# Kernel tuning notes

Measured on AMD Instinct MI355X. Metric: run time of the kernel, lower is better.

The kernel has to match this reference:

```python
import jax, jax.numpy as jnp
import numpy as np

# dims: B=batch, S=src_len, H=hidden, E=char_embed, V=vocab, L=lstm layers
B, S, H, E, V, L = 512, 64, 1024, 256, 128, 2


def setup_inputs() -> dict:
    key = jax.random.key(0)
    ks = jax.random.split(key, 20)
    def n(k, shape, scale=0.05):
        return jax.random.normal(k, shape, dtype=jnp.float32) * scale
    return {
        "input_ids": jax.random.randint(ks[0], (B, 1), 0, V),
        "hidden": n(ks[1], (L, B, H), 1.0),
        "cell": n(ks[2], (L, B, H), 1.0),
        "encoder_outputs": n(ks[3], (B, S, H), 1.0),
        "emb": n(ks[4], (V, E)),          # nn.Embedding weight
        "U": n(ks[5], (H, H)),             # attention U (applied as x @ U)
        "W": n(ks[6], (H, H)),             # attention W
        "Vw": n(ks[7], (H, 1)),            # attention V -> scalar score
        "Wih0": n(ks[8], (4 * H, E + H)),  # LSTM layer0 input weights (i,f,g,o)
        "Whh0": n(ks[9], (4 * H, H)),
        "bih0": n(ks[10], (4 * H,)),
        "bhh0": n(ks[11], (4 * H,)),
        "Wih1": n(ks[12], (4 * H, H)),     # LSTM layer1
        "Whh1": n(ks[13], (4 * H, H)),
        "bih1": n(ks[14], (4 * H,)),
        "bhh1": n(ks[15], (4 * H,)),
        "out_w": n(ks[16], (V, H)),        # output nn.Linear weight (out,in)
        "out_b": n(ks[17], (V,)),
        "matrix": 0,
    }


def _lstm_step(x, h, c, Wih, Whh, bih, bhh):
    g = x @ Wih.T + h @ Whh.T + bih + bhh          # (B, 4H), torch gate order i,f,g,o
    i, f, gg, o = jnp.split(g, 4, axis=-1)
    c2 = jax.nn.sigmoid(f) * c + jax.nn.sigmoid(i) * jnp.tanh(gg)
    h2 = jax.nn.sigmoid(o) * jnp.tanh(c2)
    return h2, c2


def reference(input_ids, hidden, cell, encoder_outputs, emb, U, W, Vw,
              Wih0, Whh0, bih0, bhh0, Wih1, Whh1, bih1, bhh1,
              out_w, out_b, matrix):
    embedded = emb[input_ids]                                  # (B,1,E)
    t1 = jnp.einsum('bsh,hk->bsk', encoder_outputs, U)         # U(enc): (B,S,H)
    t2 = hidden[-1] @ W                                        # W(h_top): (B,H)
    e = jnp.tanh(t1 + t2[:, None, :]) @ Vw                     # scores: (B,S,1)
    a = jax.nn.softmax(e, axis=1)                              # attention weights over S
    ct = jnp.einsum('bso,bsh->boh', a, encoder_outputs)        # context: (B,1,H)
    x = jnp.concatenate([embedded, ct], axis=2)[:, 0, :]       # (B, E+H); dropout p=0 -> identity
    h0, c0 = _lstm_step(x, hidden[0], cell[0], Wih0, Whh0, bih0, bhh0)
    h1, c1 = _lstm_step(h0, hidden[1], cell[1], Wih1, Whh1, bih1, bhh1)
    out = (h1 @ out_w.T + out_b)[:, None, :]                   # (B,1,V)
    h_new = jnp.stack([h0, h1])
    c_new = jnp.stack([c0, c1])
    if matrix:
        return (a, out, h_new, c_new)
    return (out, h_new, c_new)
```

## Files before the change

### kernel.cpp

```cpp
#include <hip/hip_runtime.h>
#include <stdint.h>

#define BB 512
#define SS 64
#define HH 1024
#define EE 256
#define VV 128

typedef __attribute__((ext_vector_type(8))) short bf16x8;
typedef __attribute__((ext_vector_type(4))) float f32x4;

constexpr size_t OFF_ENC   = 0;
constexpr size_t OFF_WIH0  = OFF_ENC   + 67108864UL;
constexpr size_t OFF_WHH0  = OFF_WIH0  + 10485760UL;
constexpr size_t OFF_WIH1  = OFF_WHH0  + 8388608UL;
constexpr size_t OFF_WHH1  = OFF_WIH1  + 8388608UL;
constexpr size_t OFF_OUTW  = OFF_WHH1  + 8388608UL;
constexpr size_t OFF_HID0  = OFF_OUTW  + 262144UL;
constexpr size_t OFF_HLAST = OFF_HID0  + 1048576UL;
constexpr size_t OFF_UT    = OFF_HLAST + 1048576UL;
constexpr size_t OFF_WT    = OFF_UT    + 2097152UL;
constexpr size_t OFF_T2    = OFF_WT    + 2097152UL;
constexpr size_t OFF_E     = OFF_T2    + 2097152UL;
constexpr size_t OFF_EMB   = OFF_E     + 131072UL;
constexpr size_t OFF_CT    = OFF_EMB   + 262144UL;
constexpr size_t OFF_G     = OFF_CT    + 1048576UL;
constexpr size_t OFF_H0B   = OFF_G     + 8388608UL;
constexpr size_t OFF_H1B   = OFF_H0B   + 1048576UL;

__device__ __forceinline__ unsigned short f2bf(float f) {
  unsigned int u = __float_as_uint(f);
  unsigned int r = (u + 0x7FFFu + ((u >> 16) & 1u)) >> 16;
  return (unsigned short)r;
}
__device__ __forceinline__ float bf2f(unsigned short h) {
  return __uint_as_float(((unsigned int)h) << 16);
}

__device__ __forceinline__ void gload_lds16(const void* g, void* l) {
  __builtin_amdgcn_global_load_lds(
      (const __attribute__((address_space(1))) unsigned int*)g,
      (__attribute__((address_space(3))) unsigned int*)l, 16, 0, 0);
}

__global__ void cvt_all(const float* __restrict__ enc, const float* __restrict__ Wih0,
                        const float* __restrict__ Whh0, const float* __restrict__ Wih1,
                        const float* __restrict__ Whh1, const float* __restrict__ outw,
                        const float* __restrict__ hid, char* __restrict__ ws) {
  long i = (long)blockIdx.x * 256 + threadIdx.x;
  const long stride = (long)gridDim.x * 256;
  for (; i < 13139968L; i += stride) {
    const float4* src; ushort4* dst; long j;
    if (i < 8388608L)       { src = (const float4*)enc;  dst = (ushort4*)(ws + OFF_ENC);  j = i; }
    else if (i < 9699328L)  { src = (const float4*)Wih0; dst = (ushort4*)(ws + OFF_WIH0); j = i - 8388608L; }
    else if (i < 10747904L) { src = (const float4*)Whh0; dst = (ushort4*)(ws + OFF_WHH0); j = i - 9699328L; }
    else if (i < 11796480L) { src = (const float4*)Wih1; dst = (ushort4*)(ws + OFF_WIH1); j = i - 10747904L; }
    else if (i < 12845056L) { src = (const float4*)Whh1; dst = (ushort4*)(ws + OFF_WHH1); j = i - 11796480L; }
    else if (i < 12877824L) { src = (const float4*)outw; dst = (ushort4*)(ws + OFF_OUTW); j = i - 12845056L; }
    else if (i < 13008896L) { src = (const float4*)hid;  dst = (ushort4*)(ws + OFF_HID0); j = i - 12877824L; }
    else { src = (const float4*)(hid + 524288); dst = (ushort4*)(ws + OFF_HLAST); j = i - 13008896L; }
    float4 v = src[j];
    ushort4 o;
    o.x = f2bf(v.x); o.y = f2bf(v.y); o.z = f2bf(v.z); o.w = f2bf(v.w);
    dst[j] = o;
  }
}

__global__ void transpose_cvt2(const float* __restrict__ U, const float* __restrict__ W,
                               char* __restrict__ ws) {
  __shared__ float tile[32][33];
  const float* in = blockIdx.z ? W : U;
  unsigned short* out = (unsigned short*)(ws + (blockIdx.z ? OFF_WT : OFF_UT));
  int bc = blockIdx.x * 32, br = blockIdx.y * 32;
  int tx = threadIdx.x & 31, ty = threadIdx.x >> 5;
#pragma unroll
  for (int i = 0; i < 32; i += 8)
    tile[ty + i][tx] = in[(long)(br + ty + i) * HH + bc + tx];
  __syncthreads();
#pragma unroll
  for (int i = 0; i < 32; i += 8)
    out[(long)(bc + ty + i) * HH + br + tx] = f2bf(tile[tx][ty + i]);
}

__global__ void build_xemb(const int* __restrict__ ids, const float* __restrict__ emb,
                           unsigned short* __restrict__ embb) {
  int t = blockIdx.x * 256 + threadIdx.x;
  int b = t >> 6, c4 = t & 63;
  float4 v = ((const float4*)(emb + (long)ids[b] * 256))[c4];
  ushort4 o;
  o.x = f2bf(v.x); o.y = f2bf(v.y); o.z = f2bf(v.z); o.w = f2bf(v.w);
  ((ushort4*)embb)[t] = o;
}

__global__ __launch_bounds__(256) void gemm_seg(
    const unsigned short* __restrict__ A0, int KA0,
    const unsigned short* __restrict__ A1, int KA1,
    const unsigned short* __restrict__ A2,
    const unsigned short* __restrict__ B0, int KB0,
    const unsigned short* __restrict__ B1,
    float* __restrict__ C, int N, int Ktot) {
  __shared__ alignas(128) unsigned short lA[128 * 64];
  __shared__ alignas(128) unsigned short lB[64 * 64];
  const int tid = threadIdx.x;
  const int lane = tid & 63, wid = tid >> 6;
  const int wr = wid >> 1, wc = wid & 1;
  const int fr = lane & 15, fg = lane >> 4;
  f32x4 acc[4][2] = {};
  const long rowA0 = (long)blockIdx.x * 128;
  const long rowB0 = (long)blockIdx.y * 64;
  for (int kt = 0; kt < Ktot; kt += 64) {
    const unsigned short* Ap; int ka, lda;
    if (kt < KA0)            { Ap = A0; ka = kt;             lda = KA0; }
    else if (kt < KA0 + KA1) { Ap = A1; ka = kt - KA0;       lda = KA1; }
    else                     { Ap = A2; ka = kt - KA0 - KA1; lda = 1024; }
    const unsigned short* Bp; int kb, ldb;
    if (kt < KB0) { Bp = B0; kb = kt;       ldb = KB0; }
    else          { Bp = B1; kb = kt - KB0; ldb = 1024; }
#pragma unroll
    for (int j = 0; j < 4; ++j) {
      int c = j * 256 + tid;
      int r = c >> 3, cc = c & 7;
      int sc = cc ^ ((r >> 1) & 7);
      gload_lds16(Ap + (rowA0 + r) * (long)lda + ka + sc * 8, &lA[c * 8]);
    }
#pragma unroll
    for (int j = 0; j < 2; ++j) {
      int c = j * 256 + tid;
      int r = c >> 3, cc = c & 7;
      int sc = cc ^ ((r >> 1) & 7);
      gload_lds16(Bp + (rowB0 + r) * (long)ldb + kb + sc * 8, &lB[c * 8]);
    }
    __syncthreads();
#pragma unroll
    for (int kk = 0; kk < 64; kk += 32) {
      bf16x8 af[4], bfv[2];
#pragma unroll
      for (int m = 0; m < 4; ++m) {
        int row = wr * 64 + m * 16 + fr;
        int ch = ((kk >> 3) + fg) ^ ((row >> 1) & 7);
        af[m] = *(const bf16x8*)&lA[row * 64 + ch * 8];
      }
#pragma unroll
      for (int n = 0; n < 2; ++n) {
        int row = wc * 32 + n * 16 + fr;
        int ch = ((kk >> 3) + fg) ^ ((row >> 1) & 7);
        bfv[n] = *(const bf16x8*)&lB[row * 64 + ch * 8];
      }
#pragma unroll
      for (int m = 0; m < 4; ++m)
#pragma unroll
        for (int n = 0; n < 2; ++n)
          acc[m][n] = __builtin_amdgcn_mfma_f32_16x16x32_bf16(af[m], bfv[n],
                                                              acc[m][n], 0, 0, 0);
    }
    __syncthreads();
  }
#pragma unroll
  for (int m = 0; m < 4; ++m)
#pragma unroll
    for (int n = 0; n < 2; ++n)
#pragma unroll
      for (int r = 0; r < 4; ++r) {
        long grow = rowA0 + wr * 64 + m * 16 + fg * 4 + r;
        long gcol = rowB0 + wc * 32 + n * 16 + fr;
        C[grow * N + gcol] = acc[m][n][r];
      }
}

__global__ __launch_bounds__(256) void gemm_outproj(
    const unsigned short* __restrict__ A, const unsigned short* __restrict__ Bt,
    float* __restrict__ C) {
  __shared__ alignas(128) unsigned short lA[128 * 64];
  __shared__ alignas(128) unsigned short lB[128 * 64];
  const int tid = threadIdx.x;
  const int lane = tid & 63, wid = tid >> 6;
  const int wr = wid >> 1, wc = wid & 1;
  const int fr = lane & 15, fg = lane >> 4;
  f32x4 acc[4][4] = {};
  const long rowA0 = (long)blockIdx.x * 128;
  const int k0 = blockIdx.y * 128;
  for (int kt = k0; kt < k0 + 128; kt += 64) {
#pragma unroll
    for (int j = 0; j < 4; ++j) {
      int c = j * 256 + tid;
      int r = c >> 3, cc = c & 7;
      gload_lds16(A + (rowA0 + r) * 1024 + kt + cc * 8, &lA[c * 8]);
    }
#pragma unroll
    for (int j = 0; j < 4; ++j) {
      int c = j * 256 + tid;
      int r = c >> 3, cc = c & 7;
      gload_lds16(Bt + (long)r * 1024 + kt + cc * 8, &lB[c * 8]);
    }
    __syncthreads();
#pragma unroll
    for (int kk = 0; kk < 64; kk += 32) {
      bf16x8 af[4], bfv[4];
#pragma unroll
      for (int m = 0; m < 4; ++m)
        af[m] = *(const bf16x8*)&lA[(wr * 64 + m * 16 + fr) * 64 + kk + fg * 8];
#pragma unroll
      for (int n = 0; n < 4; ++n)
        bfv[n] = *(const bf16x8*)&lB[(wc * 64 + n * 16 + fr) * 64 + kk + fg * 8];
#pragma unroll
      for (int m = 0; m < 4; ++m)
#pragma unroll
        for (int n = 0; n < 4; ++n)
          acc[m][n] = __builtin_amdgcn_mfma_f32_16x16x32_bf16(af[m], bfv[n],
                                                              acc[m][n], 0, 0, 0);
    }
    __syncthreads();
  }
#pragma unroll
  for (int m = 0; m < 4; ++m)
#pragma unroll
    for (int n = 0; n < 4; ++n)
#pragma unroll
      for (int r = 0; r < 4; ++r) {
        long grow = rowA0 + wr * 64 + m * 16 + fg * 4 + r;
        long gcol = wc * 64 + n * 16 + fr;
        atomicAdd(&C[grow * 128 + gcol], acc[m][n][r]);
      }
}

__global__ void init_out_bias(const float* __restrict__ ob, float* __restrict__ out) {
  int i = blockIdx.x * 256 + threadIdx.x;
  out[i] = ob[i & 127];
}

__global__ __launch_bounds__(512, 2) void gemm_score256(
    const unsigned short* __restrict__ A, const unsigned short* __restrict__ Bt,
    const float* __restrict__ t2, const float* __restrict__ Vw,
    float* __restrict__ e) {
  extern __shared__ unsigned short smem[];
  const int K = HH;
  const int tid = threadIdx.x;
  const int lane = tid & 63, wid = tid >> 6;
  const int wr = wid >> 2;
  const int wcc = wid & 3;
  const int fr = lane & 15, fg = lane >> 4;
  int flat = blockIdx.y * 4 + blockIdx.x;
  int swz = (flat & 7) * 64 + (flat >> 3);
  const long rowA0 = (long)(swz >> 2) * 256;
  const long rowB0 = (long)(swz & 3) * 256;
  const int NKT = 16, NIT = 8;

  f32x4 acc[8][4] = {};

  auto RA = [&](int buf, int kh) { return (const unsigned short*)(smem + (buf * 4 + kh * 2) * 8192); };
  auto RB = [&](int buf, int kh) { return (const unsigned short*)(smem + (buf * 4 + kh * 2 + 1) * 8192); };

  auto stage = [&](int buf, int reg, int ktile) {
    const unsigned short* base = (reg & 1) ? Bt : A;
    long r0 = (reg & 1) ? rowB0 : rowA0;
    int kb = ktile * 64 + (reg >> 1) * 32;
    unsigned short* dst = smem + (buf * 4 + reg) * 8192;
#pragma unroll
    for (int j = 0; j < 2; ++j) {
      int c = j * 512 + tid;
      int row = c >> 2;
      int fgl = (c & 3) ^ ((row >> 1) & 3);
      gload_lds16(base + (r0 + row) * (long)K + kb + fgl * 8, dst + c * 8);
    }
  };
  auto readA = [&](const unsigned short* rg, int mh, bf16x8* af) {
#pragma unroll
    for (int m = 0; m < 4; ++m) {
      int row = wr * 128 + mh * 64 + m * 16 + fr;
      int slot = fg ^ ((row >> 1) & 3);
      af[m] = *(const bf16x8*)(rg + row * 32 + slot * 8);
    }
  };
  auto readB = [&](const unsigned short* rg, bf16x8* bv) {
#pragma unroll
    for (int n = 0; n < 4; ++n) {
      int row = wcc * 64 + n * 16 + fr;
      int slot = fg ^ ((row >> 1) & 3);
      bv[n] = *(const bf16x8*)(rg + row * 32 + slot * 8);
    }
  };
  auto mfma16 = [&](int mh, const bf16x8* af, const bf16x8* bv) {
    __builtin_amdgcn_s_setprio(1);
#pragma unroll
    for (int m = 0; m < 4; ++m)
#pragma unroll
      for (int n = 0; n < 4; ++n)
        acc[mh * 4 + m][n] = __builtin_amdgcn_mfma_f32_16x16x32_bf16(
            af[m], bv[n], acc[mh * 4 + m][n], 0, 0, 0);
    __builtin_amdgcn_s_setprio(0);
  };

#define BAR() __builtin_amdgcn_s_barrier()
#define WAIT6() asm volatile("s_waitcnt vmcnt(6)" ::: "memory")

  bf16x8 afA[4], afB[4], bvA[4], bvB[4];

  stage(0, 0, 0); stage(0, 1, 0); stage(0, 2, 0); stage(0, 3, 0);
  stage(1, 0, 1); stage(1, 1, 1);
  asm volatile("s_waitcnt vmcnt(8)" ::: "memory");
  BAR();
  readA(RA(0, 0), 0, afA); readB(RB(0, 0), bvA);

  for (int t = 0; t < NIT; ++t) {
    int k1 = 2 * t + 1, k2 = 2 * t + 2, k3 = 2 * t + 3;
    if (k2 >= NKT) k2 -= NKT;
    if (k3 >= NKT) k3 -= NKT;
    readA(RA(0, 0), 1, afB);
    stage(1, 2, k1);
    BAR(); mfma16(0, afA, bvA); BAR();
    WAIT6();
    readA(RA(0, 1), 0, afA); readB(RB(0, 1), bvB);
    stage(1, 3, k1);
    BAR(); mfma16(1, afB, bvA); BAR();
    readA(RA(0, 1), 1, afB);
    stage(0, 0, k2);
    BAR(); mfma16(0, afA, bvB); BAR();
    WAIT6();
    readA(RA(1, 0), 0, afA); readB(RB(1, 0), bvA);
    stage(0, 1, k2);
    BAR(); mfma16(1, afB, bvB); BAR();
    readA(RA(1, 0), 1, afB);
    stage(0, 2, k2);
    BAR(); mfma16(0, afA, bvA); BAR();
    WAIT6();
    readA(RA(1, 1), 0, afA); readB(RB(1, 1), bvB);
    stage(0, 3, k2);
    BAR(); mfma16(1, afB, bvA); BAR();
    readA(RA(1, 1), 1, afB);
    stage(1, 0, k3);
    BAR(); mfma16(0, afA, bvB); BAR();
    WAIT6();
    readA(RA(0, 0), 0, afA); readB(RB(0, 0), bvA);
    stage(1, 1, k3);
    BAR(); mfma16(1, afB, bvB); BAR();
  }
  asm volatile("s_waitcnt vmcnt(0)" ::: "memory");

  float t2v[2][4], vw[4];
#pragma unroll
  for (int n = 0; n < 4; ++n) {
    long col = rowB0 + wcc * 64 + n * 16 + fr;
    vw[n] = Vw[col];
#pragma unroll
    for (int h = 0; h < 2; ++h) {
      long b = (rowA0 >> 6) + wr * 2 + h;
      t2v[h][n] = t2[b * HH + col];
    }
  }
#pragma unroll
  for (int i = 0; i < 8; ++i) {
    int hsel = i >> 2;
    float part[4] = {0.f, 0.f, 0.f, 0.f};
#pragma unroll
    for (int n = 0; n < 4; ++n) {
#pragma unroll
      for (int r = 0; r < 4; ++r) {
        float tval = acc[i][n][r] + t2v[hsel][n];
        float th = 1.f - 2.f / (__expf(2.f * tval) + 1.f);
        part[r] += th * vw[n];
      }
    }
#pragma unroll
    for (int r = 0; r < 4; ++r) {
      float p = part[r];
      p += __shfl_xor(p, 1);
      p += __shfl_xor(p, 2);
      p += __shfl_xor(p, 4);
      p += __shfl_xor(p, 8);
      if (fr == 0)
        atomicAdd(&e[rowA0 + wr * 128 + i * 16 + fg * 4 + r], p);
    }
  }
#undef BAR
#undef WAIT6
}

__global__ void softmax_ctx(const float* __restrict__ e,
                            const unsigned short* __restrict__ encb,
                            unsigned short* __restrict__ ctb) {
  __shared__ float als[2][64];
  const int tid = threadIdx.x;
  const int bpair = blockIdx.x;
  if (tid < 128) {
    int b = bpair * 2 + (tid >> 6), s = tid & 63;
    float v = e[b * 64 + s];
    float mx = v;
#pragma unroll
    for (int o = 32; o; o >>= 1) mx = fmaxf(mx, __shfl_xor(mx, o));
    float ex = __expf(v - mx);
    float sm = ex;
#pragma unroll
    for (int o = 32; o; o >>= 1) sm += __shfl_xor(sm, o);
    als[tid >> 6][s] = ex / sm;
  }
  __syncthreads();
  int bi = tid >> 7, hg = tid & 127;
  int b = bpair * 2 + bi;
  const unsigned short* er = encb + (long)b * (SS * HH) + hg * 8;
  float s[8] = {0.f, 0.f, 0.f, 0.f, 0.f, 0.f, 0.f, 0.f};
  for (int i = 0; i < 64; ++i) {
    float av = als[bi][i];
    bf16x8 v = *(const bf16x8*)(er + (long)i * HH);
#pragma unroll
    for (int j = 0; j < 8; ++j) s[j] += av * bf2f((unsigned short)v[j]);
  }
  unsigned short* dst = ctb + (long)b * HH + hg * 8;
#pragma unroll
  for (int j = 0; j < 8; ++j) dst[j] = f2bf(s[j]);
}

__global__ void lstm_cell(const float* __restrict__ g, const float* __restrict__ bih,
                          const float* __restrict__ bhh, const float* __restrict__ cin,
                          float* __restrict__ hout, float* __restrict__ cout,
                          unsigned short* __restrict__ hb) {
  int idx = blockIdx.x * 256 + threadIdx.x;
  int b = idx >> 10, h = idx & 1023;
  const float* gr = g + (long)b * 4096;
  float gi = gr[h] + bih[h] + bhh[h];
  float gf = gr[1024 + h] + bih[1024 + h] + bhh[1024 + h];
  float gg = gr[2048 + h] + bih[2048 + h] + bhh[2048 + h];
  float go = gr[3072 + h] + bih[3072 + h] + bhh[3072 + h];
  float si = 1.f / (1.f + __expf(-gi));
  float sf = 1.f / (1.f + __expf(-gf));
  float so = 1.f / (1.f + __expf(-go));
  float tg = 1.f - 2.f / (__expf(2.f * gg) + 1.f);
  float c2 = sf * cin[idx] + si * tg;
  float tc = 1.f - 2.f / (__expf(2.f * c2) + 1.f);
  float h2 = so * tc;
  cout[idx] = c2;
  hout[idx] = h2;
  hb[idx] = f2bf(h2);
}

extern "C" void kernel_launch(void* const* d_in, const int* in_sizes, int n_in,
                              void* d_out, int out_size, void* d_ws, size_t ws_size,
                              hipStream_t stream) {
  const int* ids = (const int*)d_in[0];
  const float* hidden = (const float*)d_in[1];
  const float* cell = (const float*)d_in[2];
  const float* enc = (const float*)d_in[3];
  const float* emb = (const float*)d_in[4];
  const float* U = (const float*)d_in[5];
  const float* W = (const float*)d_in[6];
  const float* Vw = (const float*)d_in[7];
  const float* Wih0 = (const float*)d_in[8];
  const float* Whh0 = (const float*)d_in[9];
  const float* bih0 = (const float*)d_in[10];
  const float* bhh0 = (const float*)d_in[11];
  const float* Wih1 = (const float*)d_in[12];
  const float* Whh1 = (const float*)d_in[13];
  const float* bih1 = (const float*)d_in[14];
  const float* bhh1 = (const float*)d_in[15];
  const float* out_w = (const float*)d_in[16];
  const float* out_b = (const float*)d_in[17];
  float* out = (float*)d_out;
  char* ws = (char*)d_ws;
  (void)in_sizes; (void)n_in; (void)out_size; (void)ws_size;

  unsigned short* enc_b  = (unsigned short*)(ws + OFF_ENC);
  unsigned short* Wih0b  = (unsigned short*)(ws + OFF_WIH0);
  unsigned short* Whh0b  = (unsigned short*)(ws + OFF_WHH0);
  unsigned short* Wih1b  = (unsigned short*)(ws + OFF_WIH1);
  unsigned short* Whh1b  = (unsigned short*)(ws + OFF_WHH1);
  unsigned short* outwb  = (unsigned short*)(ws + OFF_OUTW);
  unsigned short* hid0b  = (unsigned short*)(ws + OFF_HID0);
  unsigned short* hlastb = (unsigned short*)(ws + OFF_HLAST);
  unsigned short* Utb    = (unsigned short*)(ws + OFF_UT);
  unsigned short* Wtb    = (unsigned short*)(ws + OFF_WT);
  float*          t2     = (float*)(ws + OFF_T2);
  float*          e      = (float*)(ws + OFF_E);
  unsigned short* embb   = (unsigned short*)(ws + OFF_EMB);
  unsigned short* ctb    = (unsigned short*)(ws + OFF_CT);
  float*          g      = (float*)(ws + OFF_G);
  unsigned short* h0b    = (unsigned short*)(ws + OFF_H0B);
  unsigned short* h1b    = (unsigned short*)(ws + OFF_H1B);

  float* out_logits = out;
  float* h_new = out + BB * VV;
  float* c_new = h_new + 2 * BB * HH;

  cvt_all<<<2048, 256, 0, stream>>>(enc, Wih0, Whh0, Wih1, Whh1, out_w, hidden, ws);
  transpose_cvt2<<<dim3(32, 32, 2), 256, 0, stream>>>(U, W, ws);
  build_xemb<<<128, 256, 0, stream>>>(ids, emb, embb);
  hipMemsetAsync(e, 0, (size_t)BB * SS * 4, stream);

  gemm_seg<<<dim3(4, 16), 256, 0, stream>>>(hlastb, 1024, nullptr, 0, nullptr,
                                            Wtb, 1024, nullptr, t2, HH, 1024);

  (void)hipFuncSetAttribute(reinterpret_cast<const void*>(gemm_score256),
                            hipFuncAttributeMaxDynamicSharedMemorySize, 131072);
  gemm_score256<<<dim3(4, 128), 512, 131072, stream>>>(enc_b, Utb, t2, Vw, e);

  softmax_ctx<<<256, 256, 0, stream>>>(e, enc_b, ctb);

  gemm_seg<<<dim3(4, 64), 256, 0, stream>>>(embb, 256, ctb, 1024, hid0b,
                                            Wih0b, 1280, Whh0b, g, 4 * HH, 2304);
  lstm_cell<<<BB * HH / 256, 256, 0, stream>>>(g, bih0, bhh0, cell, h_new, c_new, h0b);

  gemm_seg<<<dim3(4, 64), 256, 0, stream>>>(h0b, 1024, hlastb, 1024, nullptr,
                                            Wih1b, 1024, Whh1b, g, 4 * HH, 2048);
  lstm_cell<<<BB * HH / 256, 256, 0, stream>>>(g, bih1, bhh1, cell + BB * HH,
                                               h_new + BB * HH, c_new + BB * HH, h1b);

  init_out_bias<<<BB * VV / 256, 256, 0, stream>>>(out_b, out_logits);
  gemm_outproj<<<dim3(4, 8), 256, 0, stream>>>(h1b, outwb, out_logits);
}
```

Baseline: 256.9 us.

## Convert LSTM weights to bf16 inside GEMM loads and split-K the LSTM GEMMs

```diff
diff --git a/kernel.cpp b/kernel.cpp
--- a/kernel.cpp
+++ b/kernel.cpp
@@ -9,13 +9,10 @@
 
 typedef __attribute__((ext_vector_type(8))) short bf16x8;
 typedef __attribute__((ext_vector_type(4))) float f32x4;
+typedef __attribute__((ext_vector_type(8))) unsigned short u16x8;
 
 constexpr size_t OFF_ENC   = 0;
-constexpr size_t OFF_WIH0  = OFF_ENC   + 67108864UL;
-constexpr size_t OFF_WHH0  = OFF_WIH0  + 10485760UL;
-constexpr size_t OFF_WIH1  = OFF_WHH0  + 8388608UL;
-constexpr size_t OFF_WHH1  = OFF_WIH1  + 8388608UL;
-constexpr size_t OFF_OUTW  = OFF_WHH1  + 8388608UL;
+constexpr size_t OFF_OUTW  = OFF_ENC   + 67108864UL;
 constexpr size_t OFF_HID0  = OFF_OUTW  + 262144UL;
 constexpr size_t OFF_HLAST = OFF_HID0  + 1048576UL;
 constexpr size_t OFF_UT    = OFF_HLAST + 1048576UL;
@@ -36,6 +33,9 @@
 __device__ __forceinline__ float bf2f(unsigned short h) {
   return __uint_as_float(((unsigned int)h) << 16);
 }
+__device__ __forceinline__ unsigned int pkbf(float a, float b) {
+  return __builtin_amdgcn_perm(__float_as_uint(b), __float_as_uint(a), 0x07060302u);
+}
 
 __device__ __forceinline__ void gload_lds16(const void* g, void* l) {
   __builtin_amdgcn_global_load_lds(
@@ -43,27 +43,28 @@
       (__attribute__((address_space(3))) unsigned int*)l, 16, 0, 0);
 }
 
-__global__ void cvt_all(const float* __restrict__ enc, const float* __restrict__ Wih0,
-                        const float* __restrict__ Whh0, const float* __restrict__ Wih1,
-                        const float* __restrict__ Whh1, const float* __restrict__ outw,
-                        const float* __restrict__ hid, char* __restrict__ ws) {
+__global__ __launch_bounds__(256) void cvt_enc(const float* __restrict__ enc,
+                                               unsigned short* __restrict__ encb) {
   long i = (long)blockIdx.x * 256 + threadIdx.x;
-  const long stride = (long)gridDim.x * 256;
-  for (; i < 13139968L; i += stride) {
-    const float4* src; ushort4* dst; long j;
-    if (i < 8388608L)       { src = (const float4*)enc;  dst = (ushort4*)(ws + OFF_ENC);  j = i; }
-    else if (i < 9699328L)  { src = (const float4*)Wih0; dst = (ushort4*)(ws + OFF_WIH0); j = i - 8388608L; }
-    else if (i < 10747904L) { src = (const float4*)Whh0; dst = (ushort4*)(ws + OFF_WHH0); j = i - 9699328L; }
-    else if (i < 11796480L) { src = (const float4*)Wih1; dst = (ushort4*)(ws + OFF_WIH1); j = i - 10747904L; }
-    else if (i < 12845056L) { src = (const float4*)Whh1; dst = (ushort4*)(ws + OFF_WHH1); j = i - 11796480L; }
-    else if (i < 12877824L) { src = (const float4*)outw; dst = (ushort4*)(ws + OFF_OUTW); j = i - 12845056L; }
-    else if (i < 13008896L) { src = (const float4*)hid;  dst = (ushort4*)(ws + OFF_HID0); j = i - 12877824L; }
-    else { src = (const float4*)(hid + 524288); dst = (ushort4*)(ws + OFF_HLAST); j = i - 13008896L; }
-    float4 v = src[j];
-    ushort4 o;
-    o.x = f2bf(v.x); o.y = f2bf(v.y); o.z = f2bf(v.z); o.w = f2bf(v.w);
-    dst[j] = o;
-  }
+  float4 v = ((const float4*)enc)[i];
+  ushort4 o;
+  o.x = f2bf(v.x); o.y = f2bf(v.y); o.z = f2bf(v.z); o.w = f2bf(v.w);
+  ((ushort4*)encb)[i] = o;
+}
+
+__global__ __launch_bounds__(256) void cvt_small(const float* __restrict__ hid,
+                                                 const float* __restrict__ outw,
+                                                 char* __restrict__ ws) {
+  int i = blockIdx.x * 256 + threadIdx.x;
+  const float4* src;
+  ushort4* dst;
+  int j;
+  if (i < 262144) { src = (const float4*)hid;  dst = (ushort4*)(ws + OFF_HID0); j = i; }
+  else            { src = (const float4*)outw; dst = (ushort4*)(ws + OFF_OUTW); j = i - 262144; }
+  float4 v = src[j];
+  ushort4 o;
+  o.x = f2bf(v.x); o.y = f2bf(v.y); o.z = f2bf(v.z); o.w = f2bf(v.w);
+  dst[j] = o;
 }
 
 __global__ void transpose_cvt2(const float* __restrict__ U, const float* __restrict__ W,
@@ -92,13 +93,13 @@
   ((ushort4*)embb)[t] = o;
 }
 
+template <int BF32>
 __global__ __launch_bounds__(256) void gemm_seg(
     const unsigned short* __restrict__ A0, int KA0,
     const unsigned short* __restrict__ A1, int KA1,
     const unsigned short* __restrict__ A2,
-    const unsigned short* __restrict__ B0, int KB0,
-    const unsigned short* __restrict__ B1,
-    float* __restrict__ C, int N, int Ktot) {
+    const void* __restrict__ B0v, int KB0, const void* __restrict__ B1v,
+    float* __restrict__ C0p, float* __restrict__ C1p, int N, int Ktot, int Khalf) {
   __shared__ alignas(128) unsigned short lA[128 * 64];
   __shared__ alignas(128) unsigned short lB[64 * 64];
   const int tid = threadIdx.x;
@@ -108,27 +109,54 @@
   f32x4 acc[4][2] = {};
   const long rowA0 = (long)blockIdx.x * 128;
   const long rowB0 = (long)blockIdx.y * 64;
-  for (int kt = 0; kt < Ktot; kt += 64) {
+  const int ktb = blockIdx.z * Khalf;
+  int kte = ktb + Khalf; if (kte > Ktot) kte = Ktot;
+  float* C = blockIdx.z ? C1p : C0p;
+  for (int kt = ktb; kt < kte; kt += 64) {
     const unsigned short* Ap; int ka, lda;
     if (kt < KA0)            { Ap = A0; ka = kt;             lda = KA0; }
     else if (kt < KA0 + KA1) { Ap = A1; ka = kt - KA0;       lda = KA1; }
     else                     { Ap = A2; ka = kt - KA0 - KA1; lda = 1024; }
-    const unsigned short* Bp; int kb, ldb;
-    if (kt < KB0) { Bp = B0; kb = kt;       ldb = KB0; }
-    else          { Bp = B1; kb = kt - KB0; ldb = 1024; }
-#pragma unroll
-    for (int j = 0; j < 4; ++j) {
-      int c = j * 256 + tid;
-      int r = c >> 3, cc = c & 7;
-      int sc = cc ^ ((r >> 1) & 7);
-      gload_lds16(Ap + (rowA0 + r) * (long)lda + ka + sc * 8, &lA[c * 8]);
-    }
-#pragma unroll
-    for (int j = 0; j < 2; ++j) {
-      int c = j * 256 + tid;
-      int r = c >> 3, cc = c & 7;
-      int sc = cc ^ ((r >> 1) & 7);
-      gload_lds16(Bp + (rowB0 + r) * (long)ldb + kb + sc * 8, &lB[c * 8]);
+    if constexpr (BF32) {
+      const float* Bp; int kb, ldb;
+      if (kt < KB0) { Bp = (const float*)B0v; kb = kt;       ldb = KB0; }
+      else          { Bp = (const float*)B1v; kb = kt - KB0; ldb = 1024; }
+      const int brow = tid >> 2, bkq = tid & 3;
+      const f32x4* bs = (const f32x4*)(Bp + (rowB0 + brow) * (long)ldb + kb) + bkq * 4;
+      f32x4 q0 = bs[0], q1 = bs[1], q2 = bs[2], q3 = bs[3];
+#pragma unroll
+      for (int j = 0; j < 4; ++j) {
+        int c = j * 256 + tid;
+        int r = c >> 3, cc = c & 7;
+        int sc = cc ^ ((r >> 1) & 7);
+        gload_lds16(Ap + (rowA0 + r) * (long)lda + ka + sc * 8, &lA[c * 8]);
+      }
+      const int bx = (brow >> 1) & 7;
+      uint4 w0, w1;
+      w0.x = pkbf(q0[0], q0[1]); w0.y = pkbf(q0[2], q0[3]);
+      w0.z = pkbf(q1[0], q1[1]); w0.w = pkbf(q1[2], q1[3]);
+      w1.x = pkbf(q2[0], q2[1]); w1.y = pkbf(q2[2], q2[3]);
+      w1.z = pkbf(q3[0], q3[1]); w1.w = pkbf(q3[2], q3[3]);
+      *(uint4*)&lB[brow * 64 + (((bkq * 2) ^ bx) * 8)] = w0;
+      *(uint4*)&lB[brow * 64 + (((bkq * 2 + 1) ^ bx) * 8)] = w1;
+    } else {
+      const unsigned short* Bp; int kb, ldb;
+      if (kt < KB0) { Bp = (const unsigned short*)B0v; kb = kt;       ldb = KB0; }
+      else          { Bp = (const unsigned short*)B1v; kb = kt - KB0; ldb = 1024; }
+#pragma unroll
+      for (int j = 0; j < 4; ++j) {
+        int c = j * 256 + tid;
+        int r = c >> 3, cc = c & 7;
+        int sc = cc ^ ((r >> 1) & 7);
+        gload_lds16(Ap + (rowA0 + r) * (long)lda + ka + sc * 8, &lA[c * 8]);
+      }
+#pragma unroll
+      for (int j = 0; j < 2; ++j) {
+        int c = j * 256 + tid;
+        int r = c >> 3, cc = c & 7;
+        int sc = cc ^ ((r >> 1) & 7);
+        gload_lds16(Bp + (rowB0 + r) * (long)ldb + kb + sc * 8, &lB[c * 8]);
+      }
     }
     __syncthreads();
 #pragma unroll
@@ -409,17 +437,19 @@
   for (int j = 0; j < 8; ++j) dst[j] = f2bf(s[j]);
 }
 
-__global__ void lstm_cell(const float* __restrict__ g, const float* __restrict__ bih,
-                          const float* __restrict__ bhh, const float* __restrict__ cin,
+__global__ void lstm_cell(const float* __restrict__ g0, const float* __restrict__ g1,
+                          const float* __restrict__ bih, const float* __restrict__ bhh,
+                          const float* __restrict__ cin,
                           float* __restrict__ hout, float* __restrict__ cout,
                           unsigned short* __restrict__ hb) {
   int idx = blockIdx.x * 256 + threadIdx.x;
   int b = idx >> 10, h = idx & 1023;
-  const float* gr = g + (long)b * 4096;
-  float gi = gr[h] + bih[h] + bhh[h];
-  float gf = gr[1024 + h] + bih[1024 + h] + bhh[1024 + h];
-  float gg = gr[2048 + h] + bih[2048 + h] + bhh[2048 + h];
-  float go = gr[3072 + h] + bih[3072 + h] + bhh[3072 + h];
+  const float* gr0 = g0 + (long)b * 4096;
+  const float* gr1 = g1 + (long)b * 4096;
+  float gi = gr0[h] + gr1[h] + bih[h] + bhh[h];
+  float gf = gr0[1024 + h] + gr1[1024 + h] + bih[1024 + h] + bhh[1024 + h];
+  float gg = gr0[2048 + h] + gr1[2048 + h] + bih[2048 + h] + bhh[2048 + h];
+  float go = gr0[3072 + h] + gr1[3072 + h] + bih[3072 + h] + bhh[3072 + h];
   float si = 1.f / (1.f + __expf(-gi));
   float sf = 1.f / (1.f + __expf(-gf));
   float so = 1.f / (1.f + __expf(-go));
@@ -458,10 +488,6 @@
   (void)in_sizes; (void)n_in; (void)out_size; (void)ws_size;
 
   unsigned short* enc_b  = (unsigned short*)(ws + OFF_ENC);
-  unsigned short* Wih0b  = (unsigned short*)(ws + OFF_WIH0);
-  unsigned short* Whh0b  = (unsigned short*)(ws + OFF_WHH0);
-  unsigned short* Wih1b  = (unsigned short*)(ws + OFF_WIH1);
-  unsigned short* Whh1b  = (unsigned short*)(ws + OFF_WHH1);
   unsigned short* outwb  = (unsigned short*)(ws + OFF_OUTW);
   unsigned short* hid0b  = (unsigned short*)(ws + OFF_HID0);
   unsigned short* hlastb = (unsigned short*)(ws + OFF_HLAST);
@@ -472,6 +498,7 @@
   unsigned short* embb   = (unsigned short*)(ws + OFF_EMB);
   unsigned short* ctb    = (unsigned short*)(ws + OFF_CT);
   float*          g      = (float*)(ws + OFF_G);
+  float*          gB     = (float*)(ws + OFF_ENC);
   unsigned short* h0b    = (unsigned short*)(ws + OFF_H0B);
   unsigned short* h1b    = (unsigned short*)(ws + OFF_H1B);
 
@@ -479,13 +506,14 @@
   float* h_new = out + BB * VV;
   float* c_new = h_new + 2 * BB * HH;
 
-  cvt_all<<<2048, 256, 0, stream>>>(enc, Wih0, Whh0, Wih1, Whh1, out_w, hidden, ws);
+  cvt_enc<<<32768, 256, 0, stream>>>(enc, enc_b);
+  cvt_small<<<1152, 256, 0, stream>>>(hidden, out_w, ws);
   transpose_cvt2<<<dim3(32, 32, 2), 256, 0, stream>>>(U, W, ws);
   build_xemb<<<128, 256, 0, stream>>>(ids, emb, embb);
   hipMemsetAsync(e, 0, (size_t)BB * SS * 4, stream);
 
-  gemm_seg<<<dim3(4, 16), 256, 0, stream>>>(hlastb, 1024, nullptr, 0, nullptr,
-                                            Wtb, 1024, nullptr, t2, HH, 1024);
+  gemm_seg<0><<<dim3(4, 16, 1), 256, 0, stream>>>(hlastb, 1024, nullptr, 0, nullptr,
+                                                  Wtb, 1024, nullptr, t2, t2, HH, 1024, 1024);
 
   (void)hipFuncSetAttribute(reinterpret_cast<const void*>(gemm_score256),
                             hipFuncAttributeMaxDynamicSharedMemorySize, 131072);
@@ -493,13 +521,13 @@
 
   softmax_ctx<<<256, 256, 0, stream>>>(e, enc_b, ctb);
 
-  gemm_seg<<<dim3(4, 64), 256, 0, stream>>>(embb, 256, ctb, 1024, hid0b,
-                                            Wih0b, 1280, Whh0b, g, 4 * HH, 2304);
-  lstm_cell<<<BB * HH / 256, 256, 0, stream>>>(g, bih0, bhh0, cell, h_new, c_new, h0b);
-
-  gemm_seg<<<dim3(4, 64), 256, 0, stream>>>(h0b, 1024, hlastb, 1024, nullptr,
-                                            Wih1b, 1024, Whh1b, g, 4 * HH, 2048);
-  lstm_cell<<<BB * HH / 256, 256, 0, stream>>>(g, bih1, bhh1, cell + BB * HH,
+  gemm_seg<1><<<dim3(4, 64, 2), 256, 0, stream>>>(embb, 256, ctb, 1024, hid0b,
+                                                  Wih0, 1280, Whh0, g, gB, 4 * HH, 2304, 1152);
+  lstm_cell<<<BB * HH / 256, 256, 0, stream>>>(g, gB, bih0, bhh0, cell, h_new, c_new, h0b);
+
+  gemm_seg<1><<<dim3(4, 64, 2), 256, 0, stream>>>(h0b, 1024, hlastb, 1024, nullptr,
+                                                  Wih1, 1024, Whh1, g, gB, 4 * HH, 2048, 1024);
+  lstm_cell<<<BB * HH / 256, 256, 0, stream>>>(g, gB, bih1, bhh1, cell + BB * HH,
                                                h_new + BB * HH, c_new + BB * HH, h1b);
 
   init_out_bias<<<BB * VV / 256, 256, 0, stream>>>(out_b, out_logits);
```

Measured after the change: 236.6 us. -7.9%, faster.
